# Performance work log

Measured on AMD Instinct MI355X. Metric: run time of the kernel, lower is better.

The kernel has to match this reference:

```python
import jax, jax.numpy as jnp
import numpy as np

GROUP_NORM_EPSILON = 1e-06
NUM_GROUPS = 32


def group_norm(x, gamma, beta, num_groups, eps):
    # x: [B, H, W, C]; normalize over (H, W, C//G) within each group.
    B, H, W, C = x.shape
    xg = x.reshape(B, H, W, num_groups, C // num_groups)
    mean = jnp.mean(xg, axis=(1, 2, 4), keepdims=True)
    var = jnp.mean(jnp.square(xg - mean), axis=(1, 2, 4), keepdims=True)
    xn = (xg - mean) * jax.lax.rsqrt(var + eps)
    return xn.reshape(B, H, W, C) * gamma + beta


def setup_inputs() -> dict:
    key = jax.random.key(0)
    ks = jax.random.split(key, 6)
    B, H, W, C = 4, 64, 64, 512
    scale = 1.0 / np.sqrt(C)
    return {
        "inputs": jax.random.normal(ks[0], (B, H, W, C), dtype=jnp.float32),
        "gamma": jnp.ones((C,), dtype=jnp.float32),
        "beta": jnp.zeros((C,), dtype=jnp.float32),
        "Wq": jax.random.normal(ks[1], (C, C), dtype=jnp.float32) * scale,
        "bq": jnp.zeros((C,), dtype=jnp.float32),
        "Wk": jax.random.normal(ks[2], (C, C), dtype=jnp.float32) * scale,
        "bk": jnp.zeros((C,), dtype=jnp.float32),
        "Wv": jax.random.normal(ks[3], (C, C), dtype=jnp.float32) * scale,
        "bv": jnp.zeros((C,), dtype=jnp.float32),
        "Wo": jax.random.normal(ks[4], (C, C), dtype=jnp.float32) * scale,
        "bo": jnp.zeros((C,), dtype=jnp.float32),
    }


def reference(inputs, gamma, beta, Wq, bq, Wk, bk, Wv, bv, Wo, bo):
    B, H, W, C = inputs.shape
    N = H * W
    h = group_norm(inputs, gamma, beta, NUM_GROUPS, GROUP_NORM_EPSILON)
    hf = h.reshape(B, N, C)  # flatten spatial: [B, N, C]
    q = hf @ Wq + bq
    k = hf @ Wk + bk
    v = hf @ Wv + bv
    # full spatial self-attention: [B, N, N]
    scores = jnp.einsum("bnc,bmc->bnm", q, k) * (C ** -0.5)
    attn = jax.nn.softmax(scores, axis=-1)
    out = jnp.einsum("bnm,bmc->bnc", attn, v)
    out = out @ Wo + bo
    return out.reshape(B, H, W, C) + inputs
```

## Files before the change

kernel.cpp:

```cpp
#include <hip/hip_runtime.h>
#include <hip/hip_bf16.h>

using bf16 = __hip_bfloat16;
using u16  = unsigned short;
typedef __attribute__((ext_vector_type(8))) short s16x8;
typedef __attribute__((ext_vector_type(4))) float f32x4;

__device__ __forceinline__ float b2f(u16 u){
  union{unsigned u; float f;} c; c.u = ((unsigned)u)<<16; return c.f;
}
__device__ __forceinline__ u16 f2b(float f){
  union{float f; unsigned u;} c; c.f = f;
  unsigned r = (c.u + 0x7FFFu + ((c.u>>16)&1u)) >> 16;
  return (u16)r;
}

#define GLDS16(g, l_) __builtin_amdgcn_global_load_lds( \
    (const __attribute__((address_space(1))) unsigned int*)(g), \
    (__attribute__((address_space(3))) unsigned int*)(l_), 16, 0, 0)

__global__ __launch_bounds__(512) void gn_kernel(const float* __restrict__ x,
    const float* __restrict__ gamma, const float* __restrict__ beta,
    bf16* __restrict__ h)
{
  const int b = blockIdx.x >> 5, g = blockIdx.x & 31;
  const int t = threadIdx.x;
  const size_t base = (size_t)b*4096*512 + (size_t)g*16;
  float sum = 0.f, sq = 0.f;
  for (int i = 0; i < 8; i++){
    const float* p = x + base + (size_t)(i*512 + t)*512;
    #pragma unroll
    for (int j = 0; j < 4; j++){
      f32x4 v = *(const f32x4*)(p + j*4);
      #pragma unroll
      for (int e = 0; e < 4; e++){ sum += v[e]; sq += v[e]*v[e]; }
    }
  }
  __shared__ float red[16];
  for (int o = 32; o > 0; o >>= 1){ sum += __shfl_xor(sum, o); sq += __shfl_xor(sq, o); }
  const int w = t >> 6, l = t & 63;
  if (l == 0){ red[w] = sum; red[8 + w] = sq; }
  __syncthreads();
  if (t == 0){
    float a = 0.f, bb = 0.f;
    for (int i = 0; i < 8; i++){ a += red[i]; bb += red[8 + i]; }
    red[0] = a; red[8] = bb;
  }
  __syncthreads();
  const float inv_n = 1.f/65536.f;
  const float mean = red[0]*inv_n;
  const float var  = red[8]*inv_n - mean*mean;
  const float rstd = rsqrtf(var + 1e-6f);
  float ga[16], be[16];
  #pragma unroll
  for (int j = 0; j < 16; j++){
    ga[j] = gamma[g*16 + j];
    be[j] = beta [g*16 + j];
  }
  u16* hp = (u16*)h;
  for (int i = 0; i < 8; i++){
    const float* p = x + base + (size_t)(i*512 + t)*512;
    u16* q = hp + base + (size_t)(i*512 + t)*512;
    s16x8 o0, o1;
    #pragma unroll
    for (int j = 0; j < 4; j++){
      f32x4 v = *(const f32x4*)(p + j*4);
      #pragma unroll
      for (int e = 0; e < 4; e++){
        int c = j*4 + e;
        u16 r = f2b((v[e] - mean)*rstd*ga[c] + be[c]);
        if (c < 8) o0[c] = (short)r; else o1[c - 8] = (short)r;
      }
    }
    *(s16x8*)q = o0; *(s16x8*)(q + 8) = o1;
  }
}

struct W4 { const float* p[4]; };
__global__ __launch_bounds__(256) void transpose_w4(W4 srcs, bf16* __restrict__ dst)
{
  __shared__ float tile[64][65];
  const float* in = srcs.p[blockIdx.z];
  u16* out = (u16*)dst + (size_t)blockIdx.z*512*512;
  const int tr = blockIdx.y*64, tc = blockIdx.x*64;
  const int t = threadIdx.x;
  #pragma unroll
  for (int i = 0; i < 16; i++){
    int idx = i*256 + t, r = idx >> 6, c = idx & 63;
    tile[r][c] = in[(size_t)(tr + r)*512 + tc + c];
  }
  __syncthreads();
  #pragma unroll
  for (int i = 0; i < 16; i++){
    int idx = i*256 + t, r = idx >> 6, c = idx & 63;
    out[(size_t)(tc + r)*512 + tr + c] = f2b(tile[c][r]);
  }
}

__global__ __launch_bounds__(256) void transpose_v(const u16* __restrict__ qkv,
    bf16* __restrict__ vT)
{
  __shared__ u16 tile[64][72];
  const u16* in = qkv + 1024 + (size_t)blockIdx.z*4096*1536;
  u16* out = (u16*)vT + (size_t)blockIdx.z*512*4096;
  const int tr = blockIdx.y*64, tc = blockIdx.x*64;
  const int t = threadIdx.x;
  #pragma unroll
  for (int i = 0; i < 16; i++){
    int idx = i*256 + t, r = idx >> 6, c = idx & 63;
    tile[r][c] = in[(size_t)(tr + r)*1536 + tc + c];
  }
  __syncthreads();
  #pragma unroll
  for (int i = 0; i < 16; i++){
    int idx = i*256 + t, r = idx >> 6, c = idx & 63;
    out[(size_t)(tc + r)*4096 + tr + c] = tile[c][r];
  }
}

template<int EPI, typename OutT>
__global__ __launch_bounds__(256) void gemm_bt(
    const u16* __restrict__ A, int lda, long sA,
    const u16* __restrict__ Bt, int ldb, long sB,
    OutT* __restrict__ Cmat, int ldc, long sC,
    int K, float scale,
    const float* __restrict__ b0, const float* __restrict__ b1,
    const float* __restrict__ b2, const float* __restrict__ res)
{
  __shared__ u16 As[128*64];
  __shared__ u16 Bs[128*64];
  const int t = threadIdx.x, l = t & 63, w = t >> 6;
  const int wr = w >> 1, wc = w & 1;
  int bx = blockIdx.x, by = blockIdx.y;
  {
    const int gx = gridDim.x, nb = gx * gridDim.y;
    if ((nb & 7) == 0){
      int lin = by*gx + bx;
      int s = (lin & 7)*(nb >> 3) + (lin >> 3);
      bx = s % gx; by = s / gx;
    }
  }
  const int m0 = by * 128, n0 = bx * 128;
  const u16* Au  = A  + (size_t)blockIdx.z * sA;
  const u16* Btu = Bt + (size_t)blockIdx.z * sB;

  f32x4 acc[4][4];
  #pragma unroll
  for (int m = 0; m < 4; m++)
    #pragma unroll
    for (int n = 0; n < 4; n++) acc[m][n] = (f32x4){0.f,0.f,0.f,0.f};

  const int srow = l >> 3;
  const int scol = ((l & 7) ^ srow) * 8;
  const int xorv = (l & 7) << 4;
  const int nkt = K >> 6;
  for (int kt = 0; kt < nkt; ++kt){
    const int k0 = kt << 6;
    #pragma unroll
    for (int j = 0; j < 4; j++){
      const int chunk = w*4 + j;
      const int row = chunk*8 + srow;
      GLDS16(Au  + (size_t)(m0 + row)*lda + k0 + scol, &As[chunk*512]);
      GLDS16(Btu + (size_t)(n0 + row)*ldb + k0 + scol, &Bs[chunk*512]);
    }
    __syncthreads();
    #pragma unroll
    for (int kk = 0; kk < 2; kk++){
      const int kbyte = (kk*64 + (l >> 4)*16) ^ xorv;
      s16x8 af[4], bff[4];
      #pragma unroll
      for (int m = 0; m < 4; m++)
        af[m]  = *(const s16x8*)((const char*)As + (wr*64 + m*16 + (l & 15))*128 + kbyte);
      #pragma unroll
      for (int n = 0; n < 4; n++)
        bff[n] = *(const s16x8*)((const char*)Bs + (wc*64 + n*16 + (l & 15))*128 + kbyte);
      #pragma unroll
      for (int m = 0; m < 4; m++)
        #pragma unroll
        for (int n = 0; n < 4; n++)
          acc[m][n] = __builtin_amdgcn_mfma_f32_16x16x32_bf16(af[m], bff[n], acc[m][n], 0, 0, 0);
    }
    __syncthreads();
  }
  const int lc = l & 15, lr4 = (l >> 4)*4;
  OutT* Cz = Cmat + (size_t)blockIdx.z * sC;
  #pragma unroll
  for (int n = 0; n < 4; n++){
    const int col = n0 + wc*64 + n*16 + lc;
    float bv = 0.f;
    if (EPI & 8){
      const float* bp = (col < 512) ? b0 : (col < 1024 ? b1 : b2);
      bv = bp[col & 511];
    } else if (EPI & 1){
      bv = b0[col];
    }
    #pragma unroll
    for (int m = 0; m < 4; m++){
      const int rowb = m0 + wr*64 + m*16 + lr4;
      #pragma unroll
      for (int r = 0; r < 4; r++){
        float v = acc[m][n][r];
        if (EPI & 2) v *= scale;
        v += bv;
        const size_t off = (size_t)(rowb + r)*ldc + col;
        if (EPI & 4) v += res[off];
        if constexpr (__is_same(OutT, float)) Cz[off] = v;
        else ((u16*)Cz)[off] = f2b(v);
      }
    }
  }
}

__global__ __launch_bounds__(512) void pv_fused(
    const u16* __restrict__ S, const u16* __restrict__ vT,
    bf16* __restrict__ ao, int batched, int batch0)
{
  __shared__ u16 Bs[256*64];
  __shared__ u16 As[64*64];
  __shared__ u16 Ps[64*64];
  __shared__ float ffarr[64];
  const int t = threadIdx.x, l = t & 63, w = t >> 6;
  int batch, mt, half;
  if (batched){
    const int lin = blockIdx.x, x = lin & 7, s = lin >> 3;
    batch = x >> 1; mt = (s >> 1)*2 + (x & 1); half = s & 1;
  } else { batch = batch0; mt = blockIdx.x >> 1; half = blockIdx.x & 1; }
  const int m0 = mt*64, c0 = half*256;
  const u16* Sb  = S  + (size_t)batch*4096*4096;
  const u16* vTb = vT + (size_t)batch*512*4096 + (size_t)c0*4096;
  u16* aob = (u16*)ao + (size_t)batch*4096*512;

  f32x4 acc[4][2];
  #pragma unroll
  for (int m = 0; m < 4; m++)
    #pragma unroll
    for (int n = 0; n < 2; n++) acc[m][n] = (f32x4){0.f,0.f,0.f,0.f};

  const int srow = l >> 3, lane8 = l & 7;
  const int scol = (lane8 ^ srow) * 8;
  const int xorv = lane8 << 4;
  const int r_loc = w*8 + srow;
  const int smaddr = r_loc*128 + ((lane8*16) ^ (srow << 4));
  float mrow = -1e30f, lsumrow = 0.f;

  for (int kt = 0; kt < 64; ++kt){
    const int k0 = kt << 6;
    #pragma unroll
    for (int j = 0; j < 4; j++){
      const int chunk = w*4 + j;
      const int row = chunk*8 + srow;
      GLDS16(vTb + (size_t)row*4096 + k0 + scol, &Bs[chunk*512]);
    }
    GLDS16(Sb + (size_t)(m0 + w*8 + srow)*4096 + k0 + scol, &As[w*512]);
    __syncthreads();

    s16x8 sv8 = *(const s16x8*)((const char*)As + smaddr);
    float f[8], lm = -1e30f;
    #pragma unroll
    for (int j = 0; j < 8; j++){ f[j] = b2f((u16)sv8[j]); lm = fmaxf(lm, f[j]); }
    lm = fmaxf(lm, __shfl_xor(lm, 1));
    lm = fmaxf(lm, __shfl_xor(lm, 2));
    lm = fmaxf(lm, __shfl_xor(lm, 4));
    float ffv = 1.f;
    if (lm - mrow > 8.f){ ffv = exp2f(mrow - lm); mrow = lm; }
    float rs = 0.f;
    s16x8 pb;
    #pragma unroll
    for (int j = 0; j < 8; j++){
      const float pvv = exp2f(f[j] - mrow);
      rs += pvv;
      pb[j] = (short)f2b(pvv);
    }
    rs += __shfl_xor(rs, 1); rs += __shfl_xor(rs, 2); rs += __shfl_xor(rs, 4);
    lsumrow = lsumrow*ffv + rs;
    if (lane8 == 0) ffarr[r_loc] = ffv;
    *(s16x8*)((char*)Ps + smaddr) = pb;
    __syncthreads();

    #pragma unroll
    for (int m = 0; m < 4; m++)
      #pragma unroll
      for (int r = 0; r < 4; r++){
        const float fD = ffarr[m*16 + (l >> 4)*4 + r];
        #pragma unroll
        for (int n = 0; n < 2; n++) acc[m][n][r] *= fD;
      }

    #pragma unroll
    for (int kk = 0; kk < 2; kk++){
      const int kbyte = (kk*64 + (l >> 4)*16) ^ xorv;
      s16x8 pa[4], bf2[2];
      #pragma unroll
      for (int m = 0; m < 4; m++)
        pa[m] = *(const s16x8*)((const char*)Ps + (m*16 + (l & 15))*128 + kbyte);
      #pragma unroll
      for (int n = 0; n < 2; n++)
        bf2[n] = *(const s16x8*)((const char*)Bs + (w*32 + n*16 + (l & 15))*128 + kbyte);
      #pragma unroll
      for (int m = 0; m < 4; m++)
        #pragma unroll
        for (int n = 0; n < 2; n++)
          acc[m][n] = __builtin_amdgcn_mfma_f32_16x16x32_bf16(pa[m], bf2[n], acc[m][n], 0, 0, 0);
    }
    __syncthreads();
  }

  if (lane8 == 0) ffarr[r_loc] = lsumrow;
  __syncthreads();
  #pragma unroll
  for (int m = 0; m < 4; m++){
    #pragma unroll
    for (int r = 0; r < 4; r++){
      const int row_loc = m*16 + (l >> 4)*4 + r;
      const float inv = 1.f / ffarr[row_loc];
      const int row = m0 + row_loc;
      #pragma unroll
      for (int n = 0; n < 2; n++){
        const int col = c0 + w*32 + n*16 + (l & 15);
        aob[(size_t)row*512 + col] = f2b(acc[m][n][r] * inv);
      }
    }
  }
}

extern "C" void kernel_launch(void* const* d_in, const int* in_sizes, int n_in,
                              void* d_out, int out_size, void* d_ws, size_t ws_size,
                              hipStream_t stream)
{
  (void)in_sizes; (void)n_in; (void)out_size;
  const float* x     = (const float*)d_in[0];
  const float* gamma = (const float*)d_in[1];
  const float* beta  = (const float*)d_in[2];
  const float* Wq = (const float*)d_in[3]; const float* bq = (const float*)d_in[4];
  const float* Wk = (const float*)d_in[5]; const float* bk = (const float*)d_in[6];
  const float* Wv = (const float*)d_in[7]; const float* bv = (const float*)d_in[8];
  const float* Wo = (const float*)d_in[9]; const float* bo = (const float*)d_in[10];
  float* out = (float*)d_out;

  const int B = 4, N = 4096, C = 512;
  const long NC = (long)N*C;
  const float scl2 = 0.04419417382415922f * 1.4426950408889634f;

  char* p0 = (char*)d_ws;
  auto align = [](size_t b){ return (b + 255) & ~(size_t)255; };
  const size_t sz_h   = align((size_t)B*NC*2);
  const size_t sz_w   = align((size_t)4*C*C*2);
  const size_t sz_qkvF= align((size_t)B*N*1536*2);
  const size_t sz_vTF = align((size_t)B*NC*2);
  const size_t sz_aoF = align((size_t)B*NC*2);
  const size_t sz_SF  = align((size_t)B*N*N*2);
  const size_t need_full = sz_h + sz_w + sz_qkvF + sz_vTF + sz_aoF + sz_SF;

  bf16* h    = (bf16*)p0;
  bf16* wAll = (bf16*)(p0 + sz_h);
  char* pv   = p0 + sz_h + sz_w;

  gn_kernel<<<dim3(B*32), dim3(512), 0, stream>>>(x, gamma, beta, h);
  W4 ws4; ws4.p[0] = Wq; ws4.p[1] = Wk; ws4.p[2] = Wv; ws4.p[3] = Wo;
  transpose_w4<<<dim3(8, 8, 4), 256, 0, stream>>>(ws4, wAll);
  bf16* woT = wAll + (size_t)3*C*C;

  if (ws_size >= need_full){
    bf16* qkv = (bf16*)pv;
    bf16* vT  = (bf16*)(pv + sz_qkvF);
    bf16* ao  = (bf16*)(pv + sz_qkvF + sz_vTF);
    bf16* S   = (bf16*)(pv + sz_qkvF + sz_vTF + sz_aoF);

    gemm_bt<8, bf16><<<dim3(12, 128, 1), 256, 0, stream>>>(
        (const u16*)h, C, 0, (const u16*)wAll, C, 0, qkv, 1536, 0,
        C, 1.f, bq, bk, bv, nullptr);
    transpose_v<<<dim3(8, 64, B), 256, 0, stream>>>((const u16*)qkv, vT);
    gemm_bt<2, bf16><<<dim3(32, 32, B), 256, 0, stream>>>(
        (const u16*)qkv, 1536, (long)N*1536, (const u16*)qkv + 512, 1536, (long)N*1536,
        S, N, (long)N*N, C, scl2, nullptr, nullptr, nullptr, nullptr);
    pv_fused<<<dim3(512), 512, 0, stream>>>(
        (const u16*)S, (const u16*)vT, ao, 1, 0);
    gemm_bt<5, float><<<dim3(4, 128, 1), 256, 0, stream>>>(
        (const u16*)ao, C, 0, (const u16*)woT, C, 0, out, C, 0,
        C, 1.f, bo, nullptr, nullptr, x);
  } else {
    const size_t sz_qkv1 = align((size_t)N*1536*2);
    const size_t sz_vT1  = align((size_t)NC*2);
    const size_t sz_ao1  = align((size_t)NC*2);
    bf16* qkv = (bf16*)pv;
    bf16* vT  = (bf16*)(pv + sz_qkv1);
    bf16* ao  = (bf16*)(pv + sz_qkv1 + sz_vT1);
    bf16* S   = (bf16*)(pv + sz_qkv1 + sz_vT1 + sz_ao1);
    for (int b = 0; b < B; b++){
      const u16* hb = (const u16*)h + (size_t)b*NC;
      gemm_bt<8, bf16><<<dim3(12, 32, 1), 256, 0, stream>>>(
          hb, C, 0, (const u16*)wAll, C, 0, qkv, 1536, 0,
          C, 1.f, bq, bk, bv, nullptr);
      transpose_v<<<dim3(8, 64, 1), 256, 0, stream>>>((const u16*)qkv, vT);
      gemm_bt<2, bf16><<<dim3(32, 32, 1), 256, 0, stream>>>(
          (const u16*)qkv, 1536, 0, (const u16*)qkv + 512, 1536, 0,
          S, N, 0, C, scl2, nullptr, nullptr, nullptr, nullptr);
      pv_fused<<<dim3(128), 512, 0, stream>>>(
          (const u16*)S, (const u16*)vT, ao, 0, b);
      gemm_bt<5, float><<<dim3(4, 32, 1), 256, 0, stream>>>(
          (const u16*)ao, C, 0, (const u16*)woT, C, 0, out + (size_t)b*NC, C, 0,
          C, 1.f, bo, nullptr, nullptr, x + (size_t)b*NC);
    }
  }
}
```

Baseline: 456.3 us.

## Prefetch score rows into registers and overlap V tile loads in PV kernel

The PV kernel no longer stages the S tile through LDS. Each thread loads its score slice straight into registers, one iteration ahead. The V tile for the next step is issued right after the MFMA barrier, and explicit waitcnt/barrier sequencing replaces one __syncthreads, so global loads overlap the softmax and MFMA work. It also skips the accumulator rescale when all correction factors are 1 and vectorizes the ffarr reads. The hand-written waitcnt counts are fragile: if the memory ordering is wrong, the kernel can race.

```diff
diff --git a/kernel.cpp b/kernel.cpp
--- a/kernel.cpp
+++ b/kernel.cpp
@@ -216,7 +216,6 @@
     bf16* __restrict__ ao, int batched, int batch0)
 {
   __shared__ u16 Bs[256*64];
-  __shared__ u16 As[64*64];
   __shared__ u16 Ps[64*64];
   __shared__ float ffarr[64];
   const int t = threadIdx.x, l = t & 63, w = t >> 6;
@@ -243,21 +242,23 @@
   const int smaddr = r_loc*128 + ((lane8*16) ^ (srow << 4));
   float mrow = -1e30f, lsumrow = 0.f;
 
+  const u16* Srow = Sb + (size_t)(m0 + r_loc)*4096 + lane8*8;
+
+  #pragma unroll
+  for (int j = 0; j < 4; j++){
+    const int chunk = w*4 + j;
+    const int row = chunk*8 + srow;
+    GLDS16(vTb + (size_t)row*4096 + scol, &Bs[chunk*512]);
+  }
+  s16x8 S_cur = *(const s16x8*)Srow;
+
   for (int kt = 0; kt < 64; ++kt){
-    const int k0 = kt << 6;
-    #pragma unroll
-    for (int j = 0; j < 4; j++){
-      const int chunk = w*4 + j;
-      const int row = chunk*8 + srow;
-      GLDS16(vTb + (size_t)row*4096 + k0 + scol, &Bs[chunk*512]);
-    }
-    GLDS16(Sb + (size_t)(m0 + w*8 + srow)*4096 + k0 + scol, &As[w*512]);
-    __syncthreads();
-
-    s16x8 sv8 = *(const s16x8*)((const char*)As + smaddr);
+    const int ktn = (kt < 63) ? kt + 1 : 63;
+    s16x8 S_next = *(const s16x8*)(Srow + ktn*64);
+
     float f[8], lm = -1e30f;
     #pragma unroll
-    for (int j = 0; j < 8; j++){ f[j] = b2f((u16)sv8[j]); lm = fmaxf(lm, f[j]); }
+    for (int j = 0; j < 8; j++){ f[j] = b2f((u16)S_cur[j]); lm = fmaxf(lm, f[j]); }
     lm = fmaxf(lm, __shfl_xor(lm, 1));
     lm = fmaxf(lm, __shfl_xor(lm, 2));
     lm = fmaxf(lm, __shfl_xor(lm, 4));
@@ -273,19 +274,33 @@
     }
     rs += __shfl_xor(rs, 1); rs += __shfl_xor(rs, 2); rs += __shfl_xor(rs, 4);
     lsumrow = lsumrow*ffv + rs;
+
+    *(s16x8*)((char*)Ps + smaddr) = pb;
     if (lane8 == 0) ffarr[r_loc] = ffv;
-    *(s16x8*)((char*)Ps + smaddr) = pb;
-    __syncthreads();
-
+
+    asm volatile("s_waitcnt lgkmcnt(0)" ::: "memory");
+    __builtin_amdgcn_sched_barrier(0);
+    asm volatile("s_waitcnt vmcnt(1)" ::: "memory");
+    __builtin_amdgcn_sched_barrier(0);
+    __builtin_amdgcn_s_barrier();
+
+    f32x4 ffq[4];
     #pragma unroll
     for (int m = 0; m < 4; m++)
-      #pragma unroll
-      for (int r = 0; r < 4; r++){
-        const float fD = ffarr[m*16 + (l >> 4)*4 + r];
+      ffq[m] = *(const f32x4*)&ffarr[m*16 + (l >> 4)*4];
+    bool anyf = false;
+    #pragma unroll
+    for (int m = 0; m < 4; m++)
+      #pragma unroll
+      for (int r = 0; r < 4; r++) anyf |= (ffq[m][r] != 1.f);
+    if (anyf){
+      #pragma unroll
+      for (int m = 0; m < 4; m++)
         #pragma unroll
-        for (int n = 0; n < 2; n++) acc[m][n][r] *= fD;
-      }
-
+        for (int r = 0; r < 4; r++)
+          #pragma unroll
+          for (int n = 0; n < 2; n++) acc[m][n][r] *= ffq[m][r];
+    }
     #pragma unroll
     for (int kk = 0; kk < 2; kk++){
       const int kbyte = (kk*64 + (l >> 4)*16) ^ xorv;
@@ -302,18 +317,29 @@
         for (int n = 0; n < 2; n++)
           acc[m][n] = __builtin_amdgcn_mfma_f32_16x16x32_bf16(pa[m], bf2[n], acc[m][n], 0, 0, 0);
     }
-    __syncthreads();
+
+    __builtin_amdgcn_sched_barrier(0);
+    __builtin_amdgcn_s_barrier();
+    __builtin_amdgcn_sched_barrier(0);
+
+    #pragma unroll
+    for (int j = 0; j < 4; j++){
+      const int chunk = w*4 + j;
+      const int row = chunk*8 + srow;
+      GLDS16(vTb + (size_t)row*4096 + ktn*64 + scol, &Bs[chunk*512]);
+    }
+    S_cur = S_next;
   }
 
   if (lane8 == 0) ffarr[r_loc] = lsumrow;
   __syncthreads();
   #pragma unroll
   for (int m = 0; m < 4; m++){
+    const f32x4 lq = *(const f32x4*)&ffarr[m*16 + (l >> 4)*4];
     #pragma unroll
     for (int r = 0; r < 4; r++){
-      const int row_loc = m*16 + (l >> 4)*4 + r;
-      const float inv = 1.f / ffarr[row_loc];
-      const int row = m0 + row_loc;
+      const float inv = 1.f / lq[r];
+      const int row = m0 + m*16 + (l >> 4)*4 + r;
       #pragma unroll
       for (int n = 0; n < 2; n++){
         const int col = c0 + w*32 + n*16 + (l & 15);
```

New measurement: 428.3 us. -6.1%, faster.
